# Performance work log

Measured on AMD Instinct MI355X. Metric: run time of the kernel, lower is better.

Reference implementation:

```python
import jax, jax.numpy as jnp
import numpy as np

N = 50000      # nodes
E = 800000     # edges
F_IN = 256
HID = [256, 256, 512]
G = 512        # graphs
FP = 2048      # fingerprint size


def setup_inputs() -> dict:
    key = jax.random.key(0)
    ks = jax.random.split(key, 14)
    node_features = jax.random.normal(ks[0], (N, F_IN), dtype=jnp.float32)
    edge_index = jax.random.randint(ks[1], (2, E), 0, N, dtype=jnp.int64)
    batch = jnp.sort(jax.random.randint(ks[2], (N,), 0, G, dtype=jnp.int64))

    def lin(k, fi, fo):
        s = 1.0 / np.sqrt(fi)
        kw, kb = jax.random.split(k)
        W = jax.random.uniform(kw, (fi, fo), jnp.float32, -s, s)
        b = jax.random.uniform(kb, (fo,), jnp.float32, -s, s)
        return W, b

    W1, b1 = lin(ks[3], F_IN, HID[0])
    W2, b2 = lin(ks[4], HID[0], HID[1])
    W3, b3 = lin(ks[5], HID[1], HID[2])
    pw, pb = lin(ks[6], HID[2], 1)          # PoolWeightedSum gating linear
    Wo, bo = lin(ks[7], 2 * HID[2], FP)     # head: weight_sum + max concat
    return dict(node_features=node_features, edge_index=edge_index, batch=batch,
                W1=W1, b1=b1, W2=W2, b2=b2, W3=W3, b3=b3,
                pw=pw, pb=pb, Wo=Wo, bo=bo)


def _gcn_layer(x, src, dst, W, b):
    # GCNConv: add self-loops, symmetric normalization, h = x @ W, aggregate.
    n = x.shape[0]
    h = x @ W  # [N, F_out]
    loop = jnp.arange(n, dtype=src.dtype)
    s = jnp.concatenate([src, loop])
    d = jnp.concatenate([dst, loop])
    deg = jax.ops.segment_sum(jnp.ones(s.shape[0], h.dtype), d, num_segments=n)
    dis = jax.lax.rsqrt(deg)  # deg >= 1 because of self-loops
    norm = dis[s] * dis[d]    # [E+N]
    out = jax.ops.segment_sum(h[s] * norm[:, None], d, num_segments=n)
    return out + b


def _forward(node_features, edge_index, batch,
             W1, b1, W2, b2, W3, b3, pw, pb, Wo, bo):
    src, dst = edge_index[0], edge_index[1]
    x = node_features
    for W, b in ((W1, b1), (W2, b2), (W3, b3)):
        x = jax.nn.relu(_gcn_layer(x, src, dst, W, b))

    # PoolWeightedSum: sigmoid-gated node features, scatter-add per graph
    w = jax.nn.sigmoid(x @ pw + pb)  # [N, 1]
    pooled_ws = jax.ops.segment_sum(x * w, batch, num_segments=G,
                                    indices_are_sorted=True)
    # PoolMax: scatter-max per graph (empty segments -> 0, like torch zeros init)
    pooled_max = jax.ops.segment_max(x, batch, num_segments=G,
                                     indices_are_sorted=True)
    pooled_max = jnp.where(jnp.isfinite(pooled_max), pooled_max, 0.0)

    feats = jnp.concatenate([pooled_ws, pooled_max], axis=1)  # [G, 2*HID[-1]]
    return jax.nn.relu(feats @ Wo + bo)  # [G, FP]


def reference(node_features, edge_index, batch,
              W1, b1, W2, b2, W3, b3, pw, pb, Wo, bo):
    return _forward(node_features, edge_index, batch,
                    W1, b1, W2, b2, W3, b3, pw, pb, Wo, bo)
```

## Files before the change

### kernel.cpp

```cpp
#include <hip/hip_runtime.h>
#include <math.h>

#define NNODES 50000
#define NEDGES 800000
#define NGRAPH 512
#define FIN    256
#define H1     256
#define H2     256
#define H3     512
#define FPOUT  2048

typedef __attribute__((ext_vector_type(8))) short short8;
typedef __attribute__((ext_vector_type(8))) _Float16 half8;
typedef __attribute__((ext_vector_type(4))) float floatx4;
typedef __attribute__((ext_vector_type(4))) unsigned short ushx4;

__device__ inline float h2f(ushort u) { return (float)__builtin_bit_cast(_Float16, u); }
__device__ inline ushort f2h(float x) { return __builtin_bit_cast(ushort, (_Float16)x); }
__device__ inline void split2h(float a, ushort& h, ushort& l) {
    _Float16 hh = (_Float16)a;
    h = __builtin_bit_cast(ushort, hh);
    l = f2h(a - (float)hh);
}


__global__ __launch_bounds__(256) void zero_i32(int* p, int n) {
    int i = blockIdx.x * 256 + threadIdx.x;
    if (i < n) p[i] = 0;
}

__global__ __launch_bounds__(256) void count_deg(const int* __restrict__ ei, int* __restrict__ degi,
                                                 int* __restrict__ rank, int e_total) {
    int e = blockIdx.x * 256 + threadIdx.x;
    if (e >= e_total) return;
    int d = ei[e_total + e];
    rank[e] = atomicAdd(&degi[d], 1);
}

__global__ __launch_bounds__(256) void calc_dis(const int* __restrict__ degi, float* __restrict__ dis, int n) {
    int i = blockIdx.x * 256 + threadIdx.x;
    if (i < n) dis[i] = rsqrtf((float)(degi[i] + 1));
}

__global__ __launch_bounds__(256) void scanA(const int* __restrict__ degi, int* __restrict__ offs,
                                             int* __restrict__ partials, int n) {
    __shared__ int sm[256];
    int t = threadIdx.x, idx = blockIdx.x * 256 + t;
    int v = (idx < n) ? degi[idx] : 0;
    sm[t] = v; __syncthreads();
    for (int d = 1; d < 256; d <<= 1) {
        int add = (t >= d) ? sm[t - d] : 0;
        __syncthreads();
        sm[t] += add;
        __syncthreads();
    }
    if (idx < n) offs[idx + 1] = sm[t];
    if (t == 255) partials[blockIdx.x] = sm[255];
}

__global__ __launch_bounds__(256) void scanB(int* __restrict__ partials, int nb) {
    __shared__ int sm[256];
    int t = threadIdx.x;
    int v = (t < nb) ? partials[t] : 0;
    sm[t] = v; __syncthreads();
    for (int d = 1; d < 256; d <<= 1) {
        int add = (t >= d) ? sm[t - d] : 0;
        __syncthreads();
        sm[t] += add;
        __syncthreads();
    }
    if (t < nb) partials[t] = sm[t] - v;
}

__global__ __launch_bounds__(256) void scanC(int* __restrict__ offs, const int* __restrict__ partials, int n) {
    int idx = blockIdx.x * 256 + threadIdx.x;
    if (idx < n) offs[idx + 1] += partials[blockIdx.x];
    if (idx == 0) offs[0] = 0;
}

__global__ __launch_bounds__(256) void fill_csr(const int* __restrict__ ei, const float* __restrict__ dis,
                                                const int* __restrict__ offs, const int* __restrict__ rank,
                                                int2* __restrict__ csr_pair, int e_total) {
    int e = blockIdx.x * 256 + threadIdx.x;
    if (e >= e_total) return;
    int s = ei[e];
    int d = ei[e_total + e];
    int pos = offs[d] + rank[e];
    int2 pr;
    pr.x = s;
    pr.y = __float_as_int(dis[s] * dis[d]);
    csr_pair[pos] = pr;
}

__global__ __launch_bounds__(256) void wsplit_t(const float* __restrict__ W, ushort* __restrict__ hi,
                                                ushort* __restrict__ lo, int K, int N) {
    __shared__ float sm[32][33];
    int tx = threadIdx.x & 31, ty = threadIdx.x >> 5;
    int n0 = blockIdx.x * 32, k0 = blockIdx.y * 32;
    #pragma unroll
    for (int j = 0; j < 32; j += 8)
        sm[ty + j][tx] = W[(size_t)(k0 + ty + j) * N + n0 + tx];
    __syncthreads();
    #pragma unroll
    for (int j = 0; j < 32; j += 8) {
        float a = sm[tx][ty + j];
        ushort h, l; split2h(a, h, l);
        size_t o = (size_t)(n0 + ty + j) * K + k0 + tx;
        hi[o] = h; lo[o] = l;
    }
}

__global__ __launch_bounds__(256) void conv_f16(const float* __restrict__ x, ushort* __restrict__ xh, int total4) {
    int i = blockIdx.x * 256 + threadIdx.x;
    if (i >= total4) return;
    float4 a = ((const float4*)x)[i];
    ushx4 h = {f2h(a.x), f2h(a.y), f2h(a.z), f2h(a.w)};
    ((ushx4*)xh)[i] = h;
}

#define LSTR 40
template<int SPLIT>
__global__ __launch_bounds__(256) void gemm_f16(const ushort* __restrict__ Ahp, const ushort* __restrict__ Alp,
                                                const ushort* __restrict__ Bhp, const ushort* __restrict__ Blp,
                                                float* __restrict__ C, ushort* __restrict__ Ch,
                                                const float* __restrict__ bias,
                                                int M, int N, int K, int do_relu, int outmode,
                                                int kspan, int accmode) {
    __shared__ _Float16 lsA[128 * LSTR];
    __shared__ _Float16 lsB[128 * LSTR];
    __shared__ _Float16 lsAl[SPLIT ? 128 * LSTR : 8];
    __shared__ _Float16 lsBl[SPLIT ? 128 * LSTR : 8];
    const _Float16* Ah = (const _Float16*)Ahp;
    const _Float16* Al = (const _Float16*)Alp;
    const _Float16* Bh = (const _Float16*)Bhp;
    const _Float16* Bl = (const _Float16*)Blp;

    int tid = threadIdx.x;
    int w = tid >> 6, lane = tid & 63;
    int quad = lane >> 4, lr = lane & 15;
    int wm = w & 1, wn = w >> 1;
    int row0 = blockIdx.y * 128, col0 = blockIdx.x * 128;
    int kb = blockIdx.z * kspan;

    floatx4 acc[4][4];
    #pragma unroll
    for (int i = 0; i < 4; ++i)
        #pragma unroll
        for (int j = 0; j < 4; ++j)
            acc[i][j] = (floatx4){0.f, 0.f, 0.f, 0.f};

    const half8 zer = {};
    int srow = tid >> 2;
    int skk  = (tid & 3) * 8;

    half8 pa[2], pb[2], pal[2], pbl[2];
    #pragma unroll
    for (int c = 0; c < 2; ++c) {
        int row = c * 64 + srow;
        bool mok = (row0 + row) < M;
        size_t aoff = (size_t)(row0 + row) * K + kb + skk;
        pa[c] = mok ? *(const half8*)(Ah + aoff) : zer;
        if constexpr (SPLIT) pal[c] = mok ? *(const half8*)(Al + aoff) : zer;
        size_t boff = (size_t)(col0 + row) * K + kb + skk;
        pb[c] = *(const half8*)(Bh + boff);
        if constexpr (SPLIT) pbl[c] = *(const half8*)(Bl + boff);
    }

    for (int k0 = kb; k0 < kb + kspan; k0 += 32) {
        #pragma unroll
        for (int c = 0; c < 2; ++c) {
            int lo = (c * 64 + srow) * LSTR + skk;
            *(half8*)(lsA + lo) = pa[c];
            *(half8*)(lsB + lo) = pb[c];
            if constexpr (SPLIT) { *(half8*)(lsAl + lo) = pal[c]; *(half8*)(lsBl + lo) = pbl[c]; }
        }
        __syncthreads();
        if (k0 + 32 < kb + kspan) {
            #pragma unroll
            for (int c = 0; c < 2; ++c) {
                int row = c * 64 + srow;
                bool mok = (row0 + row) < M;
                size_t aoff = (size_t)(row0 + row) * K + k0 + 32 + skk;
                pa[c] = mok ? *(const half8*)(Ah + aoff) : zer;
                if constexpr (SPLIT) pal[c] = mok ? *(const half8*)(Al + aoff) : zer;
                size_t boff = (size_t)(col0 + row) * K + k0 + 32 + skk;
                pb[c] = *(const half8*)(Bh + boff);
                if constexpr (SPLIT) pbl[c] = *(const half8*)(Bl + boff);
            }
        }
        half8 af[4], afl[4];
        #pragma unroll
        for (int mt = 0; mt < 4; ++mt) {
            int ao = (wm * 64 + mt * 16 + lr) * LSTR + quad * 8;
            af[mt] = *(const half8*)(lsA + ao);
            if constexpr (SPLIT) afl[mt] = *(const half8*)(lsAl + ao);
        }
        #pragma unroll
        for (int nt = 0; nt < 4; ++nt) {
            int bo = (wn * 64 + nt * 16 + lr) * LSTR + quad * 8;
            half8 bf = *(const half8*)(lsB + bo);
            half8 bfl;
            if constexpr (SPLIT) bfl = *(const half8*)(lsBl + bo);
            #pragma unroll
            for (int mt = 0; mt < 4; ++mt) {
                acc[mt][nt] = __builtin_amdgcn_mfma_f32_16x16x32_f16(af[mt], bf, acc[mt][nt], 0, 0, 0);
                if constexpr (SPLIT) {
                    acc[mt][nt] = __builtin_amdgcn_mfma_f32_16x16x32_f16(af[mt], bfl, acc[mt][nt], 0, 0, 0);
                    acc[mt][nt] = __builtin_amdgcn_mfma_f32_16x16x32_f16(afl[mt], bf, acc[mt][nt], 0, 0, 0);
                }
            }
        }
        __syncthreads();
    }

    size_t zoff = accmode ? (size_t)blockIdx.z * M * N : 0;
    #pragma unroll
    for (int mt = 0; mt < 4; ++mt) {
        #pragma unroll
        for (int r = 0; r < 4; ++r) {
            int row = row0 + wm * 64 + mt * 16 + quad * 4 + r;
            if (row >= M) continue;
            #pragma unroll
            for (int nt = 0; nt < 4; ++nt) {
                int col = col0 + wn * 64 + nt * 16 + lr;
                float v = acc[mt][nt][r];
                if (!accmode) {
                    v += bias[col];
                    if (do_relu) v = v > 0.f ? v : 0.f;
                }
                if (outmode) Ch[(size_t)row * N + col] = f2h(v);
                else         C[zoff + (size_t)row * N + col] = v;
            }
        }
    }
}

__global__ __launch_bounds__(256) void head_fin(const float* __restrict__ part, const float* __restrict__ bo,
                                                float* __restrict__ out) {
    int i4 = blockIdx.x * 256 + threadIdx.x;
    const int TOT4 = NGRAPH * FPOUT / 4;
    if (i4 >= TOT4) return;
    int col4 = i4 & (FPOUT / 4 - 1);
    const size_t STRIDE4 = (size_t)NGRAPH * FPOUT / 4;
    const float4* p = (const float4*)part;
    float4 a = p[i4];
    float4 b = p[i4 + STRIDE4];
    float4 c = p[i4 + 2 * STRIDE4];
    float4 d = p[i4 + 3 * STRIDE4];
    float4 bb = ((const float4*)bo)[col4];
    float4 o;
    o.x = a.x + b.x + c.x + d.x + bb.x; o.x = o.x > 0.f ? o.x : 0.f;
    o.y = a.y + b.y + c.y + d.y + bb.y; o.y = o.y > 0.f ? o.y : 0.f;
    o.z = a.z + b.z + c.z + d.z + bb.z; o.z = o.z > 0.f ? o.z : 0.f;
    o.w = a.w + b.w + c.w + d.w + bb.w; o.w = o.w > 0.f ? o.w : 0.f;
    ((float4*)out)[i4] = o;
}

__global__ __launch_bounds__(256) void agg256b(const ushort* __restrict__ xh, ushort* __restrict__ yh,
                                               const float* __restrict__ dis,
                                               const int* __restrict__ offs, const int2* __restrict__ csr_pair) {
    constexpr int F = 256;
    int wave = threadIdx.x >> 6;
    int lane = threadIdx.x & 63;
    int half = lane >> 5;
    int sub  = lane & 31;
    int v = blockIdx.x * 8 + wave * 2 + half;
    int beg = offs[v], end = offs[v + 1];
    int len = end - beg;
    int leno = __shfl_xor(len, 32, 64);
    int maxlen = len > leno ? len : leno;

    float dv = dis[v];
    float sw = dv * dv;
    short8 a0 = ((const short8*)(xh + (size_t)v * F))[sub];
    float acc[8];
    #pragma unroll
    for (int j = 0; j < 8; ++j) acc[j] = h2f((ushort)a0[j]) * sw;

    for (int k = 0; k < maxlen; k += 8) {
        int   s[8];
        float w[8];
        #pragma unroll
        for (int u = 0; u < 8; ++u) {
            int idx = beg + k + u;
            bool val = idx < end;
            int ic = val ? idx : beg;
            int2 pr = csr_pair[ic];
            s[u] = pr.x;
            w[u] = val ? __int_as_float(pr.y) : 0.f;
        }
        short8 g[8];
        #pragma unroll
        for (int u = 0; u < 8; ++u)
            g[u] = ((const short8*)(xh + (size_t)s[u] * F))[sub];
        #pragma unroll
        for (int u = 0; u < 8; ++u) {
            #pragma unroll
            for (int j = 0; j < 8; ++j)
                acc[j] += h2f((ushort)g[u][j]) * w[u];
        }
    }

    ushort h[8];
    #pragma unroll
    for (int j = 0; j < 8; ++j) h[j] = f2h(acc[j]);
    short8 hv = {(short)h[0], (short)h[1], (short)h[2], (short)h[3], (short)h[4], (short)h[5], (short)h[6], (short)h[7]};
    ((short8*)(yh + (size_t)v * F))[sub] = hv;
}

__global__ __launch_bounds__(256) void gatepool(const float* __restrict__ x, const float* __restrict__ pw,
                                                const float* __restrict__ pb, const int* __restrict__ batch,
                                                ushort* __restrict__ phi, ushort* __restrict__ plo, int n) {
    int g = blockIdx.x;
    int t = threadIdx.x;
    int wave = t >> 6, lane = t & 63;
    int lo_ = 0, hi_ = n;
    while (lo_ < hi_) { int mid = (lo_ + hi_) >> 1; if (batch[mid] < g) lo_ = mid + 1; else hi_ = mid; }
    int start = lo_;
    hi_ = n;
    while (lo_ < hi_) { int mid = (lo_ + hi_) >> 1; if (batch[mid] < g + 1) lo_ = mid + 1; else hi_ = mid; }
    int end = lo_;

    const float4* pwv = (const float4*)pw;
    float4 wa = pwv[lane], wb = pwv[lane + 64];
    float pb0 = pb[0];

    float4 s0 = make_float4(0.f, 0.f, 0.f, 0.f), s1 = s0;
    float4 m0 = make_float4(-INFINITY, -INFINITY, -INFINITY, -INFINITY), m1 = m0;

    for (int nn = start + wave; nn < end; nn += 4) {
        const float4* xr = (const float4*)(x + (size_t)nn * 512);
        float4 a = xr[lane];
        float4 b = xr[lane + 64];
        float p = a.x * wa.x + a.y * wa.y + a.z * wa.z + a.w * wa.w
                + b.x * wb.x + b.y * wb.y + b.z * wb.z + b.w * wb.w;
        #pragma unroll
        for (int off = 32; off; off >>= 1) p += __shfl_down(p, off, 64);
        float wg = __shfl(p, 0, 64);
        wg = 1.f / (1.f + expf(-(wg + pb0)));
        s0.x += a.x * wg; s0.y += a.y * wg; s0.z += a.z * wg; s0.w += a.w * wg;
        s1.x += b.x * wg; s1.y += b.y * wg; s1.z += b.z * wg; s1.w += b.w * wg;
        m0.x = fmaxf(m0.x, a.x); m0.y = fmaxf(m0.y, a.y); m0.z = fmaxf(m0.z, a.z); m0.w = fmaxf(m0.w, a.w);
        m1.x = fmaxf(m1.x, b.x); m1.y = fmaxf(m1.y, b.y); m1.z = fmaxf(m1.z, b.z); m1.w = fmaxf(m1.w, b.w);
    }

    __shared__ float ls[4][1024];
    *(float4*)&ls[wave][lane * 4]       = s0;
    *(float4*)&ls[wave][256 + lane * 4] = s1;
    *(float4*)&ls[wave][512 + lane * 4] = m0;
    *(float4*)&ls[wave][768 + lane * 4] = m1;
    __syncthreads();

    float sa = ls[0][t] + ls[1][t] + ls[2][t] + ls[3][t];
    float sb = ls[0][t + 256] + ls[1][t + 256] + ls[2][t + 256] + ls[3][t + 256];
    float ma = fmaxf(fmaxf(ls[0][512 + t], ls[1][512 + t]), fmaxf(ls[2][512 + t], ls[3][512 + t]));
    float mb = fmaxf(fmaxf(ls[0][768 + t], ls[1][768 + t]), fmaxf(ls[2][768 + t], ls[3][768 + t]));
    if (start >= end) { ma = 0.f; mb = 0.f; }
    ushort h, l;
    size_t base = (size_t)g * 1024;
    split2h(sa, h, l); phi[base + t] = h;       plo[base + t] = l;
    split2h(sb, h, l); phi[base + 256 + t] = h; plo[base + 256 + t] = l;
    split2h(ma, h, l); phi[base + 512 + t] = h; plo[base + 512 + t] = l;
    split2h(mb, h, l); phi[base + 768 + t] = h; plo[base + 768 + t] = l;
}


extern "C" void kernel_launch(void* const* d_in, const int* in_sizes, int n_in,
                              void* d_out, int out_size, void* d_ws, size_t ws_size,
                              hipStream_t stream) {
    const float* x0    = (const float*)d_in[0];
    const int*   ei    = (const int*)d_in[1];
    const int*   batch = (const int*)d_in[2];
    const float* W1 = (const float*)d_in[3];
    const float* b1 = (const float*)d_in[4];
    const float* W2 = (const float*)d_in[5];
    const float* b2 = (const float*)d_in[6];
    const float* W3 = (const float*)d_in[7];
    const float* b3 = (const float*)d_in[8];
    const float* pw = (const float*)d_in[9];
    const float* pb = (const float*)d_in[10];
    const float* Wo = (const float*)d_in[11];
    const float* bo = (const float*)d_in[12];
    float* out = (float*)d_out;

    float* ws = (float*)d_ws;
    size_t off = 0;
    float* bufB = ws + off; off += (size_t)NNODES * 512;
    ushort* xh  = (ushort*)(ws + off); off += (size_t)NNODES * 256 / 2;
    ushort* yh  = (ushort*)(ws + off); off += (size_t)NNODES * 256 / 2;
    int*    rank = (int*)(ws + off);   off += (size_t)NNODES * 256 / 2;
    ushort* W1thi = (ushort*)(ws + off); off += 256 * 256 / 2;
    ushort* W1tlo = (ushort*)(ws + off); off += 256 * 256 / 2;
    ushort* W2thi = (ushort*)(ws + off); off += 256 * 256 / 2;
    ushort* W2tlo = (ushort*)(ws + off); off += 256 * 256 / 2;
    ushort* W3thi = (ushort*)(ws + off); off += 512 * 256 / 2;
    ushort* W3tlo = (ushort*)(ws + off); off += 512 * 256 / 2;
    ushort* Wothi = (ushort*)(ws + off); off += (size_t)FPOUT * 1024 / 2;
    ushort* Wotlo = (ushort*)(ws + off); off += (size_t)FPOUT * 1024 / 2;
    ushort* phi = (ushort*)(ws + off); off += (size_t)NGRAPH * 1024 / 2;
    ushort* plo = (ushort*)(ws + off); off += (size_t)NGRAPH * 1024 / 2;
    float* dis  = ws + off; off += NNODES;
    int*   degi = (int*)(ws + off); off += NNODES;
    int*   offs = (int*)(ws + off); off += (NNODES + 4);
    int*   curs_unused = (int*)(ws + off); off += NNODES;
    (void)curs_unused;
    int2*  csr_pair = (int2*)(ws + off); off += 2 * (size_t)NEDGES;
    int*   partials = (int*)(ws + off); off += 256;

    const int NB_N = (NNODES + 255) / 256;
    const int NB_E = (NEDGES + 255) / 256;
    const int NB_A = NNODES / 8;
    const int MB128 = (NNODES + 127) / 128;

    { dim3 g(256 / 32, 256 / 32);    wsplit_t<<<g, 256, 0, stream>>>(W1, W1thi, W1tlo, 256, 256); }
    { dim3 g(256 / 32, 256 / 32);    wsplit_t<<<g, 256, 0, stream>>>(W2, W2thi, W2tlo, 256, 256); }
    { dim3 g(512 / 32, 256 / 32);    wsplit_t<<<g, 256, 0, stream>>>(W3, W3thi, W3tlo, 256, 512); }
    { dim3 g(FPOUT / 32, 1024 / 32); wsplit_t<<<g, 256, 0, stream>>>(Wo, Wothi, Wotlo, 1024, FPOUT); }

    zero_i32<<<NB_N, 256, 0, stream>>>(degi, NNODES);
    count_deg<<<NB_E, 256, 0, stream>>>(ei, degi, rank, NEDGES);
    calc_dis<<<NB_N, 256, 0, stream>>>(degi, dis, NNODES);
    scanA<<<NB_N, 256, 0, stream>>>(degi, offs, partials, NNODES);
    scanB<<<1, 256, 0, stream>>>(partials, NB_N);
    scanC<<<NB_N, 256, 0, stream>>>(offs, partials, NNODES);
    fill_csr<<<NB_E, 256, 0, stream>>>(ei, dis, offs, rank, csr_pair, NEDGES);

    conv_f16<<<(NNODES * 256 / 4 + 255) / 256, 256, 0, stream>>>(x0, xh, NNODES * 256 / 4);

    agg256b<<<NB_A, 256, 0, stream>>>(xh, yh, dis, offs, csr_pair);
    {
        dim3 grid(H1 / 128, MB128);
        gemm_f16<0><<<grid, 256, 0, stream>>>(yh, nullptr, W1thi, nullptr, nullptr, xh, b1,
                                              NNODES, H1, FIN, 1, 1, FIN, 0);
    }
    agg256b<<<NB_A, 256, 0, stream>>>(xh, yh, dis, offs, csr_pair);
    {
        dim3 grid(H2 / 128, MB128);
        gemm_f16<0><<<grid, 256, 0, stream>>>(yh, nullptr, W2thi, nullptr, nullptr, xh, b2,
                                              NNODES, H2, H1, 1, 1, H1, 0);
    }
    agg256b<<<NB_A, 256, 0, stream>>>(xh, yh, dis, offs, csr_pair);
    {
        dim3 grid(H3 / 128, MB128);
        gemm_f16<0><<<grid, 256, 0, stream>>>(yh, nullptr, W3thi, nullptr, bufB, nullptr, b3,
                                              NNODES, H3, H2, 1, 0, H2, 0);
    }
    gatepool<<<NGRAPH, 256, 0, stream>>>(bufB, pw, pb, batch, phi, plo, NNODES);
    {
        dim3 grid(FPOUT / 128, (NGRAPH + 127) / 128, 4);
        gemm_f16<1><<<grid, 256, 0, stream>>>(phi, plo, Wothi, Wotlo, bufB, nullptr, nullptr,
                                              NGRAPH, FPOUT, 1024, 0, 0, 256, 1);
    }
    head_fin<<<(NGRAPH * FPOUT / 4 + 255) / 256, 256, 0, stream>>>(bufB, bo, out);
}
```

Baseline: 566.2 us.

## Deepen GEMM K-tile with XOR-swizzled LDS, XCD remap, and widen gatepool

The GEMM now stages 64-wide K tiles in unpadded shared memory using an XOR swizzle in place of padding to avoid bank conflicts. The K span becomes a compile-time template parameter, and block IDs are remapped so that neighbouring tiles land on the same XCD for L2 locality. The gatepool kernel goes from 4 to 16 waves per graph, which adds parallelism for the per-graph reduction. The trade-offs are more shared memory per block (SPLIT needs 64KB) and more registers for prefetch, both of which can lower occupancy.

```diff
diff --git a/kernel.cpp b/kernel.cpp
--- a/kernel.cpp
+++ b/kernel.cpp
@@ -118,18 +118,16 @@
     ((ushx4*)xh)[i] = h;
 }
 
-#define LSTR 40
-template<int SPLIT>
+template<int SPLIT, int ACC, int KSPAN>
 __global__ __launch_bounds__(256) void gemm_f16(const ushort* __restrict__ Ahp, const ushort* __restrict__ Alp,
                                                 const ushort* __restrict__ Bhp, const ushort* __restrict__ Blp,
                                                 float* __restrict__ C, ushort* __restrict__ Ch,
                                                 const float* __restrict__ bias,
-                                                int M, int N, int K, int do_relu, int outmode,
-                                                int kspan, int accmode) {
-    __shared__ _Float16 lsA[128 * LSTR];
-    __shared__ _Float16 lsB[128 * LSTR];
-    __shared__ _Float16 lsAl[SPLIT ? 128 * LSTR : 8];
-    __shared__ _Float16 lsBl[SPLIT ? 128 * LSTR : 8];
+                                                int M, int N, int K, int do_relu, int outmode) {
+    __shared__ _Float16 lsA[128 * 64];
+    __shared__ _Float16 lsB[128 * 64];
+    __shared__ _Float16 lsAl[SPLIT ? 128 * 64 : 8];
+    __shared__ _Float16 lsBl[SPLIT ? 128 * 64 : 8];
     const _Float16* Ah = (const _Float16*)Ahp;
     const _Float16* Al = (const _Float16*)Alp;
     const _Float16* Bh = (const _Float16*)Bhp;
@@ -139,8 +137,15 @@
     int w = tid >> 6, lane = tid & 63;
     int quad = lane >> 4, lr = lane & 15;
     int wm = w & 1, wn = w >> 1;
-    int row0 = blockIdx.y * 128, col0 = blockIdx.x * 128;
-    int kb = blockIdx.z * kspan;
+
+    int gx = gridDim.x;
+    int orig = blockIdx.y * gx + blockIdx.x;
+    int nwg = gx * gridDim.y;
+    int xcd = orig & 7, slot = orig >> 3;
+    int q = nwg >> 3, r = nwg & 7;
+    int wid = (xcd < r ? xcd * (q + 1) : r * (q + 1) + (xcd - r) * q) + slot;
+    int row0 = (wid / gx) * 128, col0 = (wid % gx) * 128;
+    int kb = blockIdx.z * KSPAN;
 
     floatx4 acc[4][4];
     #pragma unroll
@@ -150,13 +155,15 @@
             acc[i][j] = (floatx4){0.f, 0.f, 0.f, 0.f};
 
     const half8 zer = {};
-    int srow = tid >> 2;
-    int skk  = (tid & 3) * 8;
-
-    half8 pa[2], pb[2], pal[2], pbl[2];
-    #pragma unroll
-    for (int c = 0; c < 2; ++c) {
-        int row = c * 64 + srow;
+    int srow = tid >> 3;
+    int sgran = tid & 7;
+    int skk = sgran * 8;
+    int sgx = (sgran ^ (srow & 7)) * 8;
+
+    half8 pa[4], pb[4], pal[4], pbl[4];
+    #pragma unroll
+    for (int c = 0; c < 4; ++c) {
+        int row = c * 32 + srow;
         bool mok = (row0 + row) < M;
         size_t aoff = (size_t)(row0 + row) * K + kb + skk;
         pa[c] = mok ? *(const half8*)(Ah + aoff) : zer;
@@ -166,65 +173,70 @@
         if constexpr (SPLIT) pbl[c] = *(const half8*)(Bl + boff);
     }
 
-    for (int k0 = kb; k0 < kb + kspan; k0 += 32) {
-        #pragma unroll
-        for (int c = 0; c < 2; ++c) {
-            int lo = (c * 64 + srow) * LSTR + skk;
+    for (int k0 = kb; k0 < kb + KSPAN; k0 += 64) {
+        #pragma unroll
+        for (int c = 0; c < 4; ++c) {
+            int lo = (c * 32 + srow) * 64 + sgx;
             *(half8*)(lsA + lo) = pa[c];
             *(half8*)(lsB + lo) = pb[c];
             if constexpr (SPLIT) { *(half8*)(lsAl + lo) = pal[c]; *(half8*)(lsBl + lo) = pbl[c]; }
         }
         __syncthreads();
-        if (k0 + 32 < kb + kspan) {
+        if (k0 + 64 < kb + KSPAN) {
             #pragma unroll
-            for (int c = 0; c < 2; ++c) {
-                int row = c * 64 + srow;
+            for (int c = 0; c < 4; ++c) {
+                int row = c * 32 + srow;
                 bool mok = (row0 + row) < M;
-                size_t aoff = (size_t)(row0 + row) * K + k0 + 32 + skk;
+                size_t aoff = (size_t)(row0 + row) * K + k0 + 64 + skk;
                 pa[c] = mok ? *(const half8*)(Ah + aoff) : zer;
                 if constexpr (SPLIT) pal[c] = mok ? *(const half8*)(Al + aoff) : zer;
-                size_t boff = (size_t)(col0 + row) * K + k0 + 32 + skk;
+                size_t boff = (size_t)(col0 + row) * K + k0 + 64 + skk;
                 pb[c] = *(const half8*)(Bh + boff);
                 if constexpr (SPLIT) pbl[c] = *(const half8*)(Bl + boff);
             }
         }
-        half8 af[4], afl[4];
-        #pragma unroll
-        for (int mt = 0; mt < 4; ++mt) {
-            int ao = (wm * 64 + mt * 16 + lr) * LSTR + quad * 8;
-            af[mt] = *(const half8*)(lsA + ao);
-            if constexpr (SPLIT) afl[mt] = *(const half8*)(lsAl + ao);
-        }
-        #pragma unroll
-        for (int nt = 0; nt < 4; ++nt) {
-            int bo = (wn * 64 + nt * 16 + lr) * LSTR + quad * 8;
-            half8 bf = *(const half8*)(lsB + bo);
-            half8 bfl;
-            if constexpr (SPLIT) bfl = *(const half8*)(lsBl + bo);
+        #pragma unroll
+        for (int kk = 0; kk < 2; ++kk) {
+            half8 af[4], afl[4];
             #pragma unroll
             for (int mt = 0; mt < 4; ++mt) {
-                acc[mt][nt] = __builtin_amdgcn_mfma_f32_16x16x32_f16(af[mt], bf, acc[mt][nt], 0, 0, 0);
-                if constexpr (SPLIT) {
-                    acc[mt][nt] = __builtin_amdgcn_mfma_f32_16x16x32_f16(af[mt], bfl, acc[mt][nt], 0, 0, 0);
-                    acc[mt][nt] = __builtin_amdgcn_mfma_f32_16x16x32_f16(afl[mt], bf, acc[mt][nt], 0, 0, 0);
+                int row = wm * 64 + mt * 16 + lr;
+                int ao = row * 64 + (((kk * 4 + quad) ^ (row & 7)) << 3);
+                af[mt] = *(const half8*)(lsA + ao);
+                if constexpr (SPLIT) afl[mt] = *(const half8*)(lsAl + ao);
+            }
+            #pragma unroll
+            for (int nt = 0; nt < 4; ++nt) {
+                int row = wn * 64 + nt * 16 + lr;
+                int bo = row * 64 + (((kk * 4 + quad) ^ (row & 7)) << 3);
+                half8 bf = *(const half8*)(lsB + bo);
+                half8 bfl;
+                if constexpr (SPLIT) bfl = *(const half8*)(lsBl + bo);
+                #pragma unroll
+                for (int mt = 0; mt < 4; ++mt) {
+                    acc[mt][nt] = __builtin_amdgcn_mfma_f32_16x16x32_f16(af[mt], bf, acc[mt][nt], 0, 0, 0);
+                    if constexpr (SPLIT) {
+                        acc[mt][nt] = __builtin_amdgcn_mfma_f32_16x16x32_f16(af[mt], bfl, acc[mt][nt], 0, 0, 0);
+                        acc[mt][nt] = __builtin_amdgcn_mfma_f32_16x16x32_f16(afl[mt], bf, acc[mt][nt], 0, 0, 0);
+                    }
                 }
             }
         }
         __syncthreads();
     }
 
-    size_t zoff = accmode ? (size_t)blockIdx.z * M * N : 0;
+    size_t zoff = ACC ? (size_t)blockIdx.z * M * N : 0;
     #pragma unroll
     for (int mt = 0; mt < 4; ++mt) {
         #pragma unroll
-        for (int r = 0; r < 4; ++r) {
-            int row = row0 + wm * 64 + mt * 16 + quad * 4 + r;
+        for (int rr = 0; rr < 4; ++rr) {
+            int row = row0 + wm * 64 + mt * 16 + quad * 4 + rr;
             if (row >= M) continue;
             #pragma unroll
             for (int nt = 0; nt < 4; ++nt) {
                 int col = col0 + wn * 64 + nt * 16 + lr;
-                float v = acc[mt][nt][r];
-                if (!accmode) {
+                float v = acc[mt][nt][rr];
+                if (!ACC) {
                     v += bias[col];
                     if (do_relu) v = v > 0.f ? v : 0.f;
                 }
@@ -308,9 +320,9 @@
     ((short8*)(yh + (size_t)v * F))[sub] = hv;
 }
 
-__global__ __launch_bounds__(256) void gatepool(const float* __restrict__ x, const float* __restrict__ pw,
-                                                const float* __restrict__ pb, const int* __restrict__ batch,
-                                                ushort* __restrict__ phi, ushort* __restrict__ plo, int n) {
+__global__ __launch_bounds__(1024) void gatepool(const float* __restrict__ x, const float* __restrict__ pw,
+                                                 const float* __restrict__ pb, const int* __restrict__ batch,
+                                                 ushort* __restrict__ phi, ushort* __restrict__ plo, int n) {
     int g = blockIdx.x;
     int t = threadIdx.x;
     int wave = t >> 6, lane = t & 63;
@@ -328,7 +340,7 @@
     float4 s0 = make_float4(0.f, 0.f, 0.f, 0.f), s1 = s0;
     float4 m0 = make_float4(-INFINITY, -INFINITY, -INFINITY, -INFINITY), m1 = m0;
 
-    for (int nn = start + wave; nn < end; nn += 4) {
+    for (int nn = start + wave; nn < end; nn += 16) {
         const float4* xr = (const float4*)(x + (size_t)nn * 512);
         float4 a = xr[lane];
         float4 b = xr[lane + 64];
@@ -344,24 +356,31 @@
         m1.x = fmaxf(m1.x, b.x); m1.y = fmaxf(m1.y, b.y); m1.z = fmaxf(m1.z, b.z); m1.w = fmaxf(m1.w, b.w);
     }
 
-    __shared__ float ls[4][1024];
+    __shared__ float ls[16][1024];
     *(float4*)&ls[wave][lane * 4]       = s0;
     *(float4*)&ls[wave][256 + lane * 4] = s1;
     *(float4*)&ls[wave][512 + lane * 4] = m0;
     *(float4*)&ls[wave][768 + lane * 4] = m1;
     __syncthreads();
 
-    float sa = ls[0][t] + ls[1][t] + ls[2][t] + ls[3][t];
-    float sb = ls[0][t + 256] + ls[1][t + 256] + ls[2][t + 256] + ls[3][t + 256];
-    float ma = fmaxf(fmaxf(ls[0][512 + t], ls[1][512 + t]), fmaxf(ls[2][512 + t], ls[3][512 + t]));
-    float mb = fmaxf(fmaxf(ls[0][768 + t], ls[1][768 + t]), fmaxf(ls[2][768 + t], ls[3][768 + t]));
-    if (start >= end) { ma = 0.f; mb = 0.f; }
+    float val;
+    if (t < 512) {
+        float s = 0.f;
+        #pragma unroll
+        for (int wv = 0; wv < 16; ++wv) s += ls[wv][t];
+        val = s;
+    } else {
+        float m = -INFINITY;
+        #pragma unroll
+        for (int wv = 0; wv < 16; ++wv) m = fmaxf(m, ls[wv][t]);
+        if (start >= end) m = 0.f;
+        val = m;
+    }
     ushort h, l;
+    split2h(val, h, l);
     size_t base = (size_t)g * 1024;
-    split2h(sa, h, l); phi[base + t] = h;       plo[base + t] = l;
-    split2h(sb, h, l); phi[base + 256 + t] = h; plo[base + 256 + t] = l;
-    split2h(ma, h, l); phi[base + 512 + t] = h; plo[base + 512 + t] = l;
-    split2h(mb, h, l); phi[base + 768 + t] = h; plo[base + 768 + t] = l;
+    phi[base + t] = h;
+    plo[base + t] = l;
 }
 
 
@@ -430,26 +449,26 @@
     agg256b<<<NB_A, 256, 0, stream>>>(xh, yh, dis, offs, csr_pair);
     {
         dim3 grid(H1 / 128, MB128);
-        gemm_f16<0><<<grid, 256, 0, stream>>>(yh, nullptr, W1thi, nullptr, nullptr, xh, b1,
-                                              NNODES, H1, FIN, 1, 1, FIN, 0);
+        gemm_f16<0, 0, 256><<<grid, 256, 0, stream>>>(yh, nullptr, W1thi, nullptr, nullptr, xh, b1,
+                                                      NNODES, H1, FIN, 1, 1);
     }
     agg256b<<<NB_A, 256, 0, stream>>>(xh, yh, dis, offs, csr_pair);
     {
         dim3 grid(H2 / 128, MB128);
-        gemm_f16<0><<<grid, 256, 0, stream>>>(yh, nullptr, W2thi, nullptr, nullptr, xh, b2,
-                                              NNODES, H2, H1, 1, 1, H1, 0);
+        gemm_f16<0, 0, 256><<<grid, 256, 0, stream>>>(yh, nullptr, W2thi, nullptr, nullptr, xh, b2,
+                                                      NNODES, H2, H1, 1, 1);
     }
     agg256b<<<NB_A, 256, 0, stream>>>(xh, yh, dis, offs, csr_pair);
     {
         dim3 grid(H3 / 128, MB128);
-        gemm_f16<0><<<grid, 256, 0, stream>>>(yh, nullptr, W3thi, nullptr, bufB, nullptr, b3,
-                                              NNODES, H3, H2, 1, 0, H2, 0);
-    }
-    gatepool<<<NGRAPH, 256, 0, stream>>>(bufB, pw, pb, batch, phi, plo, NNODES);
+        gemm_f16<0, 0, 256><<<grid, 256, 0, stream>>>(yh, nullptr, W3thi, nullptr, bufB, nullptr, b3,
+                                                      NNODES, H3, H2, 1, 0);
+    }
+    gatepool<<<NGRAPH, 1024, 0, stream>>>(bufB, pw, pb, batch, phi, plo, NNODES);
     {
         dim3 grid(FPOUT / 128, (NGRAPH + 127) / 128, 4);
-        gemm_f16<1><<<grid, 256, 0, stream>>>(phi, plo, Wothi, Wotlo, bufB, nullptr, nullptr,
-                                              NGRAPH, FPOUT, 1024, 0, 0, 256, 1);
+        gemm_f16<1, 1, 256><<<grid, 256, 0, stream>>>(phi, plo, Wothi, Wotlo, bufB, nullptr, nullptr,
+                                                      NGRAPH, FPOUT, 1024, 0, 0);
     }
     head_fin<<<(NGRAPH * FPOUT / 4 + 255) / 256, 256, 0, stream>>>(bufB, bo, out);
 }
```

Result: faster. 528.1 us (-6.7%).
